# Optimization experiments

Measured on AMD Instinct MI355X. Metric: run time of the kernel, lower is better.

Reference implementation:

```python
import jax, jax.numpy as jnp
import numpy as np

EMB = 64
N_CONS = 100000
N_VARS = 200000
N_EDGES = 2000000


def _embed(x, shift, scale, W1, b1, W2, b2):
    # PreNormLayer (affine) -> Linear -> ReLU -> Linear -> ReLU
    x = (x - shift) * scale
    x = jax.nn.relu(x @ W1 + b1)
    return jax.nn.relu(x @ W2 + b2)


def _biconv(left, right, ei0, ei1, edge_lin, tgt_idx, n_tgt, tgt_feats,
            Wl, bl, Wr, sf, Wf, bf, sp, Woa, boa, Wob, bob):
    # gather-transform: per-edge joint features [E, EMB]
    joint = (left @ Wl + bl)[ei0] + edge_lin + (right @ Wr)[ei1]
    # feature_module_final: PreNorm(scale-only) -> ReLU -> Linear
    msg = jax.nn.relu(joint * sf) @ Wf + bf
    # scatter-add to target nodes, then post-conv PreNorm(scale-only)
    agg = jax.ops.segment_sum(msg, tgt_idx, num_segments=n_tgt) * sp
    h = jax.nn.relu(jnp.concatenate([agg, tgt_feats], axis=1) @ Woa + boa)
    return h @ Wob + bob


def _forward(constraint_features, edge_features, variable_features,
             c_shift, c_scale, c_W1, c_b1, c_W2, c_b2,
             v_shift, v_scale, v_W1, v_b1, v_W2, v_b2,
             e_shift, e_scale,
             vc_Wl, vc_bl, vc_We, vc_Wr, vc_sf, vc_Wf, vc_bf, vc_sp,
             vc_Woa, vc_boa, vc_Wob, vc_bob,
             cv_Wl, cv_bl, cv_We, cv_Wr, cv_sf, cv_Wf, cv_bf, cv_sp,
             cv_Woa, cv_boa, cv_Wob, cv_bob,
             out_W1, out_b1, out_W2, edge_indices):
    ei0, ei1 = edge_indices[0], edge_indices[1]
    c = _embed(constraint_features, c_shift, c_scale, c_W1, c_b1, c_W2, c_b2)
    v = _embed(variable_features, v_shift, v_scale, v_W1, v_b1, v_W2, v_b2)
    e = (edge_features - e_shift) * e_scale  # edge embedding = PreNorm only, dim 1
    # conv_v_to_c (right_to_left=True): target = constraints via ei0
    c = jax.nn.relu(_biconv(c, v, ei0, ei1, e @ vc_We, ei0, N_CONS, c,
                            vc_Wl, vc_bl, vc_Wr, vc_sf, vc_Wf, vc_bf, vc_sp,
                            vc_Woa, vc_boa, vc_Wob, vc_bob))
    # conv_c_to_v: target = variables via ei1
    v = jax.nn.relu(_biconv(c, v, ei0, ei1, e @ cv_We, ei1, N_VARS, v,
                            cv_Wl, cv_bl, cv_Wr, cv_sf, cv_Wf, cv_bf, cv_sp,
                            cv_Woa, cv_boa, cv_Wob, cv_bob))
    out = jax.nn.relu(v @ out_W1 + out_b1) @ out_W2  # [N_VARS, 1]
    return out.reshape(1, -1)


def setup_inputs():
    key = jax.random.key(0)
    ks = iter(jax.random.split(key, 64))

    def rn(shape, s=0.1):
        return (jax.random.normal(next(ks), shape, jnp.float32) * s).astype(jnp.float32)

    d = {}
    d["constraint_features"] = rn((N_CONS, 5), 1.0)
    d["edge_features"] = rn((N_EDGES, 1), 1.0)
    d["variable_features"] = rn((N_VARS, 19), 1.0)

    def prenorm(n, pre):
        d[pre + "shift"] = rn((n,), 0.05)
        d[pre + "scale"] = jnp.ones((n,), jnp.float32) + rn((n,), 0.05)

    prenorm(5, "c_"); prenorm(19, "v_"); prenorm(1, "e_")
    for pre, nin in (("c_", 5), ("v_", 19)):
        d[pre + "W1"] = rn((nin, EMB)); d[pre + "b1"] = rn((EMB,), 0.02)
        d[pre + "W2"] = rn((EMB, EMB)); d[pre + "b2"] = rn((EMB,), 0.02)
    for pre in ("vc_", "cv_"):
        d[pre + "Wl"] = rn((EMB, EMB)); d[pre + "bl"] = rn((EMB,), 0.02)
        d[pre + "We"] = rn((1, EMB)); d[pre + "Wr"] = rn((EMB, EMB))
        d[pre + "sf"] = jnp.float32(1.0) + rn((), 0.05)
        d[pre + "Wf"] = rn((EMB, EMB)); d[pre + "bf"] = rn((EMB,), 0.02)
        d[pre + "sp"] = jnp.float32(1.0) + rn((), 0.05)
        d[pre + "Woa"] = rn((2 * EMB, EMB)); d[pre + "boa"] = rn((EMB,), 0.02)
        d[pre + "Wob"] = rn((EMB, EMB)); d[pre + "bob"] = rn((EMB,), 0.02)
    d["out_W1"] = rn((EMB, EMB)); d["out_b1"] = rn((EMB,), 0.02)
    d["out_W2"] = rn((EMB, 1))
    d["edge_indices"] = jnp.stack([
        jax.random.randint(next(ks), (N_EDGES,), 0, N_CONS),
        jax.random.randint(next(ks), (N_EDGES,), 0, N_VARS)]).astype(jnp.int32)
    d["n_cons_per_sample"] = jnp.array([N_CONS], jnp.int32)
    d["n_vars_per_sample"] = jnp.array([N_VARS], jnp.int32)
    return d


def reference(constraint_features, edge_features, variable_features,
              c_shift, c_scale, c_W1, c_b1, c_W2, c_b2,
              v_shift, v_scale, v_W1, v_b1, v_W2, v_b2,
              e_shift, e_scale,
              vc_Wl, vc_bl, vc_We, vc_Wr, vc_sf, vc_Wf, vc_bf, vc_sp,
              vc_Woa, vc_boa, vc_Wob, vc_bob,
              cv_Wl, cv_bl, cv_We, cv_Wr, cv_sf, cv_Wf, cv_bf, cv_sp,
              cv_Woa, cv_boa, cv_Wob, cv_bob,
              out_W1, out_b1, out_W2,
              edge_indices, n_cons_per_sample, n_vars_per_sample):
    return _forward(constraint_features, edge_features, variable_features,
                    c_shift, c_scale, c_W1, c_b1, c_W2, c_b2,
                    v_shift, v_scale, v_W1, v_b1, v_W2, v_b2,
                    e_shift, e_scale,
                    vc_Wl, vc_bl, vc_We, vc_Wr, vc_sf, vc_Wf, vc_bf, vc_sp,
                    vc_Woa, vc_boa, vc_Wob, vc_bob,
                    cv_Wl, cv_bl, cv_We, cv_Wr, cv_sf, cv_Wf, cv_bf, cv_sp,
                    cv_Woa, cv_boa, cv_Wob, cv_bob,
                    out_W1, out_b1, out_W2, edge_indices)
```

## Files before the change

kernel.cpp:

```cpp
#include <hip/hip_runtime.h>
#include <hip/hip_bf16.h>

#define DEV __device__ __forceinline__

typedef __attribute__((ext_vector_type(8))) short short8;
typedef __attribute__((ext_vector_type(4))) float f32x4;

DEV unsigned short f2bf(float f) {
    __hip_bfloat16 h = __float2bfloat16(f);
    unsigned short u;
    __builtin_memcpy(&u, &h, 2);
    return u;
}
DEV float bf2f(unsigned short u) { return __uint_as_float((unsigned int)u << 16); }

DEV f32x4 mfma_bf16(short8 a, short8 b, f32x4 c) {
    return __builtin_amdgcn_mfma_f32_16x16x32_bf16(a, b, c, 0, 0, 0);
}

DEV void make_hilo(const float* a8, short8& hi, short8& lo) {
    #pragma unroll
    for (int j = 0; j < 8; ++j) {
        const float v = a8[j];
        const unsigned short h = f2bf(v);
        hi[j] = (short)h;
        lo[j] = (short)f2bf(v - bf2f(h));
    }
}

DEV void mfma3(f32x4 acc[4], short8 ah, short8 al,
               const unsigned short* __restrict__ Bh,
               const unsigned short* __restrict__ Bl,
               int nkt, int tidx, int lane) {
    #pragma unroll
    for (int c = 0; c < 4; ++c) {
        const size_t o = ((size_t)(c * nkt + tidx) * 64 + lane) * 8;
        const short8 bh = *(const short8*)(Bh + o);
        const short8 bl = *(const short8*)(Bl + o);
        acc[c] = mfma_bf16(ah, bh, acc[c]);
        acc[c] = mfma_bf16(al, bh, acc[c]);
        acc[c] = mfma_bf16(ah, bl, acc[c]);
    }
}

DEV int swf(int row, int col) {
    return row * 64 + ((((col >> 3) ^ row) & 7) << 3) + (col & 7);
}

DEV void gemm_lds(f32x4 acc[4], const float* Xl,
                  const unsigned short* Bh, const unsigned short* Bl,
                  int nkt, int t0, int ntk, int l15, int q, int lane) {
    for (int t = 0; t < ntk; ++t) {
        const int ch = (t * 4 + q) ^ (l15 & 7);
        const float* a8 = Xl + l15 * 64 + ch * 8;
        short8 ah, al;
        make_hilo(a8, ah, al);
        mfma3(acc, ah, al, Bh, Bl, nkt, t0 + t, lane);
    }
}

DEV void gemm_glb(f32x4 acc[4], const float* __restrict__ Xg, int rbase, int N,
                  const unsigned short* Bh, const unsigned short* Bl,
                  int nkt, int t0, int ntk, int l15, int q, int lane) {
    const int grow = rbase + l15;
    const bool ok = grow < N;
    for (int t = 0; t < ntk; ++t) {
        float a8[8];
        if (ok) {
            const float4 v0 = *(const float4*)(Xg + (size_t)grow * 64 + t * 32 + q * 8);
            const float4 v1 = *(const float4*)(Xg + (size_t)grow * 64 + t * 32 + q * 8 + 4);
            a8[0] = v0.x; a8[1] = v0.y; a8[2] = v0.z; a8[3] = v0.w;
            a8[4] = v1.x; a8[5] = v1.y; a8[6] = v1.z; a8[7] = v1.w;
        } else {
            #pragma unroll
            for (int j = 0; j < 8; ++j) a8[j] = 0.f;
        }
        short8 ah, al;
        make_hilo(a8, ah, al);
        mfma3(acc, ah, al, Bh, Bl, nkt, t0 + t, lane);
    }
}

#define NMAT 15
struct PrepArgs {
    const float* src[NMAT];
    unsigned short* hi[NMAT];
    unsigned short* lo[NMAT];
    int nkt[NMAT];
    int KR[NMAT];
};

__global__ __launch_bounds__(256)
void prep_kernel(PrepArgs pa)
{
    const int m = blockIdx.y;
    const int nkt = pa.nkt[m];
    const int nthr = nkt * 4 * 64;
    const int p = blockIdx.x * 256 + threadIdx.x;
    if (p >= nthr) return;
    const int f = p >> 6, l = p & 63;
    const int c = f / nkt, t = f % nkt;
    const int kbase = t * 32 + ((l >> 4) << 3);
    const int n = c * 16 + (l & 15);
    const float* W = pa.src[m];
    const int KR = pa.KR[m];
    unsigned short* ph = pa.hi[m] + (size_t)p * 8;
    unsigned short* pl = pa.lo[m] + (size_t)p * 8;
    #pragma unroll
    for (int j = 0; j < 8; ++j) {
        const int k = kbase + j;
        const float v = (k < KR) ? W[k * 64 + n] : 0.f;
        const unsigned short h = f2bf(v);
        ph[j] = h;
        pl[j] = f2bf(v - bf2f(h));
    }
}

struct FusedArgs {
    const int* ei; int E; int nH;
    int* h1; int* h2; unsigned int* rank;
    int tC, tV;
    const float* cf; int NC;
    const float* c_shift; const float* c_scale;
    const float* vf; int NV;
    const float* v_shift; const float* v_scale;
    const unsigned short *cW1h, *cW1l, *cW2h, *cW2l, *cWt1h, *cWt1l;
    const unsigned short *vW1h, *vW1l, *vW2h, *vW2l, *vWt1h, *vWt1l, *vWt2h, *vWt2l;
    const float *c_b1, *c_b2, *v_b1, *v_b2, *vc_bl;
    const float *vc_sf, *cv_sf;
    float* Emc; float* Emv;
    unsigned short* A1; unsigned short* B1; unsigned short* B2;
};

__global__ __launch_bounds__(256)
void fused_he_kernel(FusedArgs a)
{
    __shared__ __align__(16) float Bb[4][1024];

    const int half = blockIdx.x & 1;
    const int idx  = blockIdx.x >> 1;

    if (half == 0) {
        const int stride = a.nH * 256;
        for (int e = idx * 256 + (int)threadIdx.x; e < a.E; e += stride) {
            const int r1 = atomicAdd(a.h1 + a.ei[e], 1);
            const int r2 = atomicAdd(a.h2 + a.ei[a.E + e], 1);
            a.rank[e] = (unsigned int)r1 | ((unsigned int)r2 << 16);
        }
        return;
    }

    int tile = idx;
    const float* x; int N; int IN;
    const float *shift, *scale, *b1, *b2, *bt1;
    const unsigned short *W1h, *W1l, *W2h, *W2l, *Wt1h, *Wt1l;
    const unsigned short *Wt2h = nullptr, *Wt2l = nullptr;
    float* Em; unsigned short* T1; unsigned short* T2 = nullptr;
    float sf1, sf2 = 0.f;
    if (tile < a.tC) {
        x = a.cf; N = a.NC; IN = 5; shift = a.c_shift; scale = a.c_scale;
        W1h = a.cW1h; W1l = a.cW1l; b1 = a.c_b1;
        W2h = a.cW2h; W2l = a.cW2l; b2 = a.c_b2;
        Em = a.Emc; Wt1h = a.cWt1h; Wt1l = a.cWt1l; bt1 = a.vc_bl;
        sf1 = a.vc_sf[0]; T1 = a.A1;
    } else {
        tile -= a.tC;
        x = a.vf; N = a.NV; IN = 19; shift = a.v_shift; scale = a.v_scale;
        W1h = a.vW1h; W1l = a.vW1l; b1 = a.v_b1;
        W2h = a.vW2h; W2l = a.vW2l; b2 = a.v_b2;
        Em = a.Emv; Wt1h = a.vWt1h; Wt1l = a.vWt1l; bt1 = nullptr;
        sf1 = a.vc_sf[0]; T1 = a.B1;
        Wt2h = a.vWt2h; Wt2l = a.vWt2l; sf2 = a.cv_sf[0]; T2 = a.B2;
    }

    const int w = threadIdx.x >> 6, lane = threadIdx.x & 63;
    const int l15 = lane & 15, q = lane >> 4;
    const int rbase = tile * 64 + w * 16;

    {
        f32x4 acc[4] = {{0,0,0,0},{0,0,0,0},{0,0,0,0},{0,0,0,0}};
        const int grow = rbase + l15;
        float a8[8];
        #pragma unroll
        for (int j = 0; j < 8; ++j) {
            const int col = q * 8 + j;
            float v = 0.f;
            if (grow < N && col < IN) v = (x[(size_t)grow * IN + col] - shift[col]) * scale[col];
            a8[j] = v;
        }
        short8 ah, al;
        make_hilo(a8, ah, al);
        mfma3(acc, ah, al, W1h, W1l, 1, 0, lane);
        #pragma unroll
        for (int c = 0; c < 4; ++c) {
            const int col = c * 16 + l15;
            const float bb = b1[col];
            #pragma unroll
            for (int r = 0; r < 4; ++r)
                Bb[w][swf(q * 4 + r, col)] = fmaxf(acc[c][r] + bb, 0.f);
        }
    }
    {
        f32x4 acc[4] = {{0,0,0,0},{0,0,0,0},{0,0,0,0},{0,0,0,0}};
        gemm_lds(acc, Bb[w], W2h, W2l, 2, 0, 2, l15, q, lane);
        #pragma unroll
        for (int c = 0; c < 4; ++c) {
            const int col = c * 16 + l15;
            const float bb = b2[col];
            #pragma unroll
            for (int r = 0; r < 4; ++r) {
                const int row = q * 4 + r;
                const int grow = rbase + row;
                const float v = fmaxf(acc[c][r] + bb, 0.f);
                Bb[w][swf(row, col)] = v;
                if (grow < N) Em[(size_t)grow * 64 + col] = v;
            }
        }
    }
    {
        f32x4 acc[4] = {{0,0,0,0},{0,0,0,0},{0,0,0,0},{0,0,0,0}};
        gemm_lds(acc, Bb[w], Wt1h, Wt1l, 2, 0, 2, l15, q, lane);
        #pragma unroll
        for (int c = 0; c < 4; ++c) {
            const int col = c * 16 + l15;
            const float bb = bt1 ? bt1[col] : 0.f;
            #pragma unroll
            for (int r = 0; r < 4; ++r) {
                const int grow = rbase + q * 4 + r;
                if (grow < N) T1[(size_t)grow * 64 + col] = f2bf(sf1 * (acc[c][r] + bb));
            }
        }
    }
    if (T2 != nullptr) {
        f32x4 acc[4] = {{0,0,0,0},{0,0,0,0},{0,0,0,0},{0,0,0,0}};
        gemm_lds(acc, Bb[w], Wt2h, Wt2l, 2, 0, 2, l15, q, lane);
        #pragma unroll
        for (int c = 0; c < 4; ++c) {
            const int col = c * 16 + l15;
            #pragma unroll
            for (int r = 0; r < 4; ++r) {
                const int grow = rbase + q * 4 + r;
                if (grow < N) T2[(size_t)grow * 64 + col] = f2bf(sf2 * acc[c][r]);
            }
        }
    }
}

template<bool IS_POST2>
__global__ __launch_bounds__(256)
void post_mfma(int N, const float* __restrict__ G, const int* __restrict__ rs,
               const float* __restrict__ Em,
               const unsigned short* __restrict__ Wfh, const unsigned short* __restrict__ Wfl,
               const float* __restrict__ bfv, const float* __restrict__ spp,
               const unsigned short* __restrict__ Woah, const unsigned short* __restrict__ Woal,
               const float* __restrict__ boa,
               const unsigned short* __restrict__ Wobh, const unsigned short* __restrict__ Wobl,
               const float* __restrict__ bob,
               const unsigned short* __restrict__ W4h, const unsigned short* __restrict__ W4l,
               const float* __restrict__ b4,
               const float* __restrict__ sf2p, unsigned short* __restrict__ A2,
               const float* __restrict__ oW2, float* __restrict__ out)
{
    __shared__ __align__(16) float BA[4][1024];
    __shared__ __align__(16) float BB[4][1024];

    const int w = threadIdx.x >> 6, lane = threadIdx.x & 63;
    const int l15 = lane & 15, q = lane >> 4;
    const float sp = spp[0];
    const float sf2 = IS_POST2 ? 0.f : sf2p[0];
    const int rbase = blockIdx.x * 64 + w * 16;

    {
        f32x4 acc[4] = {{0,0,0,0},{0,0,0,0},{0,0,0,0},{0,0,0,0}};
        gemm_glb(acc, G, rbase, N, Wfh, Wfl, 2, 0, 2, l15, q, lane);
        float dgr[4];
        #pragma unroll
        for (int r = 0; r < 4; ++r) {
            const int grow = rbase + q * 4 + r;
            dgr[r] = (grow < N) ? (float)(rs[grow + 1] - rs[grow]) : 0.f;
        }
        #pragma unroll
        for (int c = 0; c < 4; ++c) {
            const int col = c * 16 + l15;
            const float bb = bfv[col];
            #pragma unroll
            for (int r = 0; r < 4; ++r)
                BA[w][swf(q * 4 + r, col)] = (acc[c][r] + dgr[r] * bb) * sp;
        }
    }
    {
        f32x4 acc[4] = {{0,0,0,0},{0,0,0,0},{0,0,0,0},{0,0,0,0}};
        gemm_lds(acc, BA[w], Woah, Woal, 4, 0, 2, l15, q, lane);
        gemm_glb(acc, Em, rbase, N, Woah, Woal, 4, 2, 2, l15, q, lane);
        #pragma unroll
        for (int c = 0; c < 4; ++c) {
            const int col = c * 16 + l15;
            const float bb = boa[col];
            #pragma unroll
            for (int r = 0; r < 4; ++r)
                BB[w][swf(q * 4 + r, col)] = fmaxf(acc[c][r] + bb, 0.f);
        }
    }
    {
        f32x4 acc[4] = {{0,0,0,0},{0,0,0,0},{0,0,0,0},{0,0,0,0}};
        gemm_lds(acc, BB[w], Wobh, Wobl, 2, 0, 2, l15, q, lane);
        #pragma unroll
        for (int c = 0; c < 4; ++c) {
            const int col = c * 16 + l15;
            const float bb = bob[col];
            #pragma unroll
            for (int r = 0; r < 4; ++r)
                BA[w][swf(q * 4 + r, col)] = fmaxf(acc[c][r] + bb, 0.f);
        }
    }
    {
        f32x4 acc[4] = {{0,0,0,0},{0,0,0,0},{0,0,0,0},{0,0,0,0}};
        gemm_lds(acc, BA[w], W4h, W4l, 2, 0, 2, l15, q, lane);
        if (!IS_POST2) {
            #pragma unroll
            for (int c = 0; c < 4; ++c) {
                const int col = c * 16 + l15;
                const float bb = b4[col];
                #pragma unroll
                for (int r = 0; r < 4; ++r) {
                    const int grow = rbase + q * 4 + r;
                    if (grow < N) A2[(size_t)grow * 64 + col] = f2bf(sf2 * (acc[c][r] + bb));
                }
            }
        } else {
            float w2c[4], bb4[4];
            #pragma unroll
            for (int c = 0; c < 4; ++c) {
                const int col = c * 16 + l15;
                w2c[c] = oW2[col];
                bb4[c] = b4[col];
            }
            #pragma unroll
            for (int r = 0; r < 4; ++r) {
                float s = 0.f;
                #pragma unroll
                for (int c = 0; c < 4; ++c)
                    s += fmaxf(acc[c][r] + bb4[c], 0.f) * w2c[c];
                s += __shfl_xor(s, 1);
                s += __shfl_xor(s, 2);
                s += __shfl_xor(s, 4);
                s += __shfl_xor(s, 8);
                const int grow = rbase + q * 4 + r;
                if (l15 == 0 && grow < N) out[grow] = s;
            }
        }
    }
}

__global__ __launch_bounds__(256)
void scanA2_kernel(const int* __restrict__ h1, int n1, int* __restrict__ cs1,
                   const int* __restrict__ h2, int n2, int* __restrict__ cs2)
{
    __shared__ int wsum[4];
    const int which = blockIdx.y;
    const int* h = which ? h2 : h1;
    const int n = which ? n2 : n1;
    int* csum = which ? cs2 : cs1;
    if (blockIdx.x * 4096 >= n) return;

    const int t = threadIdx.x, lane = t & 63, wid = t >> 6;
    const int base = blockIdx.x * 4096 + t * 16;
    int s = 0;
    #pragma unroll
    for (int j = 0; j < 16; ++j) {
        const int idx = base + j;
        if (idx < n) s += h[idx];
    }
    #pragma unroll
    for (int d = 1; d < 64; d <<= 1) s += __shfl_xor(s, d);
    if (lane == 0) wsum[wid] = s;
    __syncthreads();
    if (t == 0) csum[blockIdx.x] = wsum[0] + wsum[1] + wsum[2] + wsum[3];
}

__global__ __launch_bounds__(256)
void scanB2_kernel(int* __restrict__ cs1, int nch1, int* __restrict__ rs1, int n1,
                   int* __restrict__ cs2, int nch2, int* __restrict__ rs2, int n2)
{
    __shared__ int wsum[4];
    const int which = blockIdx.x;
    int* csum = which ? cs2 : cs1;
    const int nchunks = which ? nch2 : nch1;
    int* rs = which ? rs2 : rs1;
    const int n = which ? n2 : n1;

    const int t = threadIdx.x, lane = t & 63, wid = t >> 6;
    const int v = (t < nchunks) ? csum[t] : 0;
    int x = v;
    #pragma unroll
    for (int d = 1; d < 64; d <<= 1) { int y = __shfl_up(x, d); if (lane >= d) x += y; }
    if (lane == 63) wsum[wid] = x;
    __syncthreads();
    int woff = 0;
    for (int i = 0; i < wid; ++i) woff += wsum[i];
    if (t < nchunks) csum[t] = woff + x - v;
    if (t == 0) rs[n] = wsum[0] + wsum[1] + wsum[2] + wsum[3];
}

__global__ __launch_bounds__(256)
void scanC2_kernel(const int* __restrict__ h1, int n1, const int* __restrict__ cs1,
                   int* __restrict__ rs1,
                   const int* __restrict__ h2, int n2, const int* __restrict__ cs2,
                   int* __restrict__ rs2)
{
    __shared__ int wsum[4];
    const int which = blockIdx.y;
    const int* h = which ? h2 : h1;
    const int n = which ? n2 : n1;
    const int* csum = which ? cs2 : cs1;
    int* rs = which ? rs2 : rs1;
    if (blockIdx.x * 4096 >= n) return;

    const int t = threadIdx.x, lane = t & 63, wid = t >> 6;
    const int base = blockIdx.x * 4096 + t * 16;
    int loc[16];
    int s = 0;
    #pragma unroll
    for (int j = 0; j < 16; ++j) {
        loc[j] = s;
        const int idx = base + j;
        if (idx < n) s += h[idx];
    }
    int x = s;
    #pragma unroll
    for (int d = 1; d < 64; d <<= 1) { int y = __shfl_up(x, d); if (lane >= d) x += y; }
    if (lane == 63) wsum[wid] = x;
    __syncthreads();
    int woff = 0;
    for (int i = 0; i < wid; ++i) woff += wsum[i];
    const int toff = csum[blockIdx.x] + woff + x - s;
    #pragma unroll
    for (int j = 0; j < 16; ++j) {
        const int idx = base + j;
        if (idx < n) rs[idx] = toff + loc[j];
    }
}

__global__ __launch_bounds__(256)
void scatter_kernel(const int* __restrict__ ei, int E,
                    const unsigned int* __restrict__ rank,
                    const int* __restrict__ rs1, const int* __restrict__ rs2,
                    unsigned int* __restrict__ items1,
                    unsigned int* __restrict__ items2)
{
    const int e = blockIdx.x * 256 + threadIdx.x;
    if (e >= E) return;
    const int i0 = ei[e];
    const int i1 = ei[E + e];
    const unsigned int rk = rank[e];
    const int pos1 = rs1[i0] + (int)(rk & 0xffffu);
    const int pos2 = rs2[i1] + (int)(rk >> 16);
    items1[pos1] = (unsigned int)e;
    items2[pos2] = (unsigned int)e;
}

DEV void agg_body(int row, int j, const int* __restrict__ rs,
                  const unsigned int* __restrict__ items,
                  const int* __restrict__ oth, const float* __restrict__ ef,
                  float esh, float esc,
                  const unsigned short* __restrict__ Ttgt,
                  const unsigned short* __restrict__ Tsrc,
                  const float* __restrict__ We, const float* __restrict__ sfp,
                  float* __restrict__ G)
{
    const float base = bf2f(Ttgt[(size_t)row * 64 + j]);
    const float sfWe = sfp[0] * We[j];
    const int s = rs[row];
    const int e = rs[row + 1];
    float acc = 0.f;
    int p = s;
    for (; p + 7 < e; p += 8) {
        unsigned int id[8];
        #pragma unroll
        for (int u = 0; u < 8; ++u) id[u] = items[p + u];
        int o[8];
        float en[8];
        #pragma unroll
        for (int u = 0; u < 8; ++u) o[u] = oth[id[u]];
        #pragma unroll
        for (int u = 0; u < 8; ++u) en[u] = (ef[id[u]] - esh) * esc;
        float b[8];
        #pragma unroll
        for (int u = 0; u < 8; ++u) b[u] = bf2f(Tsrc[(size_t)o[u] * 64 + j]);
        #pragma unroll
        for (int u = 0; u < 8; ++u)
            acc += fmaxf(base + b[u] + en[u] * sfWe, 0.f);
    }
    for (; p < e; ++p) {
        const unsigned int id = items[p];
        const int o = oth[id];
        const float en = (ef[id] - esh) * esc;
        const float bs = bf2f(Tsrc[(size_t)o * 64 + j]);
        acc += fmaxf(base + bs + en * sfWe, 0.f);
    }
    G[(size_t)row * 64 + j] = acc;
}

__global__ __launch_bounds__(256)
void agg_kernel(int nrows, const int* __restrict__ rs,
                const unsigned int* __restrict__ items,
                const int* __restrict__ oth, const float* __restrict__ ef,
                const float* __restrict__ eshp, const float* __restrict__ escp,
                const unsigned short* __restrict__ Ttgt,
                const unsigned short* __restrict__ Tsrc,
                const float* __restrict__ We, const float* __restrict__ sfp,
                float* __restrict__ G)
{
    const int row = blockIdx.x * 4 + (int)(threadIdx.x >> 6);
    if (row >= nrows) return;
    agg_body(row, (int)(threadIdx.x & 63), rs, items, oth, ef,
             eshp[0], escp[0], Ttgt, Tsrc, We, sfp, G);
}

extern "C" void kernel_launch(void* const* d_in, const int* in_sizes, int n_in,
                              void* d_out, int out_size, void* d_ws, size_t ws_size,
                              hipStream_t stream)
{
    const float* cf      = (const float*)d_in[0];
    const float* ef      = (const float*)d_in[1];
    const float* vf      = (const float*)d_in[2];
    const float* c_shift = (const float*)d_in[3];
    const float* c_scale = (const float*)d_in[4];
    const float* v_shift = (const float*)d_in[5];
    const float* v_scale = (const float*)d_in[6];
    const float* e_shift = (const float*)d_in[7];
    const float* e_scale = (const float*)d_in[8];
    const float* c_W1 = (const float*)d_in[9];
    const float* c_b1 = (const float*)d_in[10];
    const float* c_W2 = (const float*)d_in[11];
    const float* c_b2 = (const float*)d_in[12];
    const float* v_W1 = (const float*)d_in[13];
    const float* v_b1 = (const float*)d_in[14];
    const float* v_W2 = (const float*)d_in[15];
    const float* v_b2 = (const float*)d_in[16];
    const float* vc_Wl  = (const float*)d_in[17];
    const float* vc_bl  = (const float*)d_in[18];
    const float* vc_We  = (const float*)d_in[19];
    const float* vc_Wr  = (const float*)d_in[20];
    const float* vc_sf  = (const float*)d_in[21];
    const float* vc_Wf  = (const float*)d_in[22];
    const float* vc_bf  = (const float*)d_in[23];
    const float* vc_sp  = (const float*)d_in[24];
    const float* vc_Woa = (const float*)d_in[25];
    const float* vc_boa = (const float*)d_in[26];
    const float* vc_Wob = (const float*)d_in[27];
    const float* vc_bob = (const float*)d_in[28];
    const float* cv_Wl  = (const float*)d_in[29];
    const float* cv_bl  = (const float*)d_in[30];
    const float* cv_We  = (const float*)d_in[31];
    const float* cv_Wr  = (const float*)d_in[32];
    const float* cv_sf  = (const float*)d_in[33];
    const float* cv_Wf  = (const float*)d_in[34];
    const float* cv_bf  = (const float*)d_in[35];
    const float* cv_sp  = (const float*)d_in[36];
    const float* cv_Woa = (const float*)d_in[37];
    const float* cv_boa = (const float*)d_in[38];
    const float* cv_Wob = (const float*)d_in[39];
    const float* cv_bob = (const float*)d_in[40];
    const float* out_W1 = (const float*)d_in[41];
    const float* out_b1 = (const float*)d_in[42];
    const float* out_W2 = (const float*)d_in[43];
    const int*   eidx   = (const int*)d_in[44];

    const int NC = in_sizes[0] / 5;
    const int NV = in_sizes[2] / 19;
    const int E  = in_sizes[1];

    char* ws = (char*)d_ws;
    size_t off = 0;
    auto alloc = [&](size_t bytes) -> size_t {
        size_t o = off;
        off = (off + bytes + 255) & ~(size_t)255;
        return o;
    };
    size_t o_h1 = alloc((size_t)NC * 4);
    size_t o_h2 = alloc((size_t)NV * 4);
    size_t zero_bytes = off;
    size_t o_rs1  = alloc((size_t)(NC + 1) * 4);
    size_t o_rs2  = alloc((size_t)(NV + 1) * 4);
    size_t o_cs1  = alloc(256 * 4);
    size_t o_cs2  = alloc(256 * 4);
    size_t o_p1   = alloc((size_t)E * 4);
    size_t o_p2   = alloc((size_t)E * 4);
    size_t o_G1   = alloc((size_t)NC * 64 * 4);
    size_t o_G2   = alloc((size_t)NV * 64 * 4);
    size_t o_Emc  = alloc((size_t)NC * 64 * 4);
    size_t o_Emv  = alloc((size_t)NV * 64 * 4);
    size_t o_A1   = alloc((size_t)NC * 64 * 2);
    size_t o_B1   = alloc((size_t)NV * 64 * 2);
    size_t o_B2   = alloc((size_t)NV * 64 * 2);

    static const int nkt_arr[NMAT] = {1,2,2,1,2,2,2,2,4,2,2,2,4,2,2};
    static const int KR_arr[NMAT]  = {5,64,64,19,64,64,64,64,128,64,64,64,128,64,64};
    const float* src_arr[NMAT] = {c_W1, c_W2, vc_Wl, v_W1, v_W2, vc_Wr, cv_Wr,
                                  vc_Wf, vc_Woa, vc_Wob, cv_Wl,
                                  cv_Wf, cv_Woa, cv_Wob, out_W1};
    size_t o_wh[NMAT], o_wl[NMAT];
    for (int m = 0; m < NMAT; ++m) {
        o_wh[m] = alloc((size_t)nkt_arr[m] * 4 * 64 * 8 * 2);
        o_wl[m] = alloc((size_t)nkt_arr[m] * 4 * 64 * 8 * 2);
    }
    (void)ws_size; (void)n_in; (void)out_size;

    int*  h1   = (int*)(ws + o_h1);
    int*  h2   = (int*)(ws + o_h2);
    int*  rs1  = (int*)(ws + o_rs1);
    int*  rs2  = (int*)(ws + o_rs2);
    int*  cs1  = (int*)(ws + o_cs1);
    int*  cs2  = (int*)(ws + o_cs2);
    unsigned int* rank = (unsigned int*)(ws + o_G2);
    unsigned int* p1 = (unsigned int*)(ws + o_p1);
    unsigned int* p2 = (unsigned int*)(ws + o_p2);
    float* G1  = (float*)(ws + o_G1);
    float* G2  = (float*)(ws + o_G2);
    float* Emc = (float*)(ws + o_Emc);
    float* Emv = (float*)(ws + o_Emv);
    unsigned short* A1 = (unsigned short*)(ws + o_A1);
    unsigned short* B1 = (unsigned short*)(ws + o_B1);
    unsigned short* A2 = (unsigned short*)(ws + o_A1);
    unsigned short* B2 = (unsigned short*)(ws + o_B2);

    PrepArgs pa;
    for (int m = 0; m < NMAT; ++m) {
        pa.src[m] = src_arr[m];
        pa.hi[m] = (unsigned short*)(ws + o_wh[m]);
        pa.lo[m] = (unsigned short*)(ws + o_wl[m]);
        pa.nkt[m] = nkt_arr[m];
        pa.KR[m] = KR_arr[m];
    }
    auto WH = [&](int m) { return (const unsigned short*)(ws + o_wh[m]); };
    auto WL = [&](int m) { return (const unsigned short*)(ws + o_wl[m]); };

    hipMemsetAsync(ws, 0, zero_bytes, stream);

    prep_kernel<<<dim3(4, NMAT), 256, 0, stream>>>(pa);

    const int tC = (NC + 63) >> 6, tV = (NV + 63) >> 6;
    const int nE = tC + tV;
    FusedArgs fa;
    fa.ei = eidx; fa.E = E; fa.nH = nE;
    fa.h1 = h1; fa.h2 = h2; fa.rank = rank;
    fa.tC = tC; fa.tV = tV;
    fa.cf = cf; fa.NC = NC; fa.c_shift = c_shift; fa.c_scale = c_scale;
    fa.vf = vf; fa.NV = NV; fa.v_shift = v_shift; fa.v_scale = v_scale;
    fa.cW1h = WH(0); fa.cW1l = WL(0); fa.cW2h = WH(1); fa.cW2l = WL(1);
    fa.cWt1h = WH(2); fa.cWt1l = WL(2);
    fa.vW1h = WH(3); fa.vW1l = WL(3); fa.vW2h = WH(4); fa.vW2l = WL(4);
    fa.vWt1h = WH(5); fa.vWt1l = WL(5); fa.vWt2h = WH(6); fa.vWt2l = WL(6);
    fa.c_b1 = c_b1; fa.c_b2 = c_b2; fa.v_b1 = v_b1; fa.v_b2 = v_b2;
    fa.vc_bl = vc_bl; fa.vc_sf = vc_sf; fa.cv_sf = cv_sf;
    fa.Emc = Emc; fa.Emv = Emv; fa.A1 = A1; fa.B1 = B1; fa.B2 = B2;
    fused_he_kernel<<<2 * nE, 256, 0, stream>>>(fa);

    const int nch1 = (NC + 4095) / 4096, nch2 = (NV + 4095) / 4096;
    const int nchm = nch1 > nch2 ? nch1 : nch2;
    scanA2_kernel<<<dim3(nchm, 2), 256, 0, stream>>>(h1, NC, cs1, h2, NV, cs2);
    scanB2_kernel<<<2, 256, 0, stream>>>(cs1, nch1, rs1, NC, cs2, nch2, rs2, NV);
    scanC2_kernel<<<dim3(nchm, 2), 256, 0, stream>>>(h1, NC, cs1, rs1, h2, NV, cs2, rs2);

    scatter_kernel<<<(E + 255) / 256, 256, 0, stream>>>(
        eidx, E, rank, rs1, rs2, p1, p2);

    agg_kernel<<<(NC + 3) / 4, 256, 0, stream>>>(
        NC, rs1, p1, eidx + E, ef, e_shift, e_scale, A1, B1, vc_We, vc_sf, G1);
    post_mfma<false><<<tC, 256, 0, stream>>>(
        NC, G1, rs1, Emc,
        WH(7), WL(7), vc_bf, vc_sp,
        WH(8), WL(8), vc_boa,
        WH(9), WL(9), vc_bob,
        WH(10), WL(10), cv_bl,
        cv_sf, A2, nullptr, nullptr);

    agg_kernel<<<(NV + 3) / 4, 256, 0, stream>>>(
        NV, rs2, p2, eidx, ef, e_shift, e_scale, B2, A2, cv_We, cv_sf, G2);
    post_mfma<true><<<tV, 256, 0, stream>>>(
        NV, G2, rs2, Emv,
        WH(11), WL(11), cv_bf, cv_sp,
        WH(12), WL(12), cv_boa,
        WH(13), WL(13), cv_bob,
        WH(14), WL(14), out_b1,
        nullptr, nullptr, out_W2, (float*)d_out);
}
```

Measured before the change: 749.7 us.

## Fuse edge aggregation into post-conv MFMA kernel, eliminating G intermediate buffers

Merges the per-row gather/ReLU aggregation into the post-convolution MFMA kernel, writing aggregated rows directly into LDS instead of a global fp32 G buffer. This removes the global write and re-read of the aggregation buffers and two kernel launches. Each wave now loops over its 16 rows sequentially for the gather, which may reduce latency hiding compared with one row per wave across many blocks. The rank buffer gets its own allocation instead of aliasing G2.

After: 1.008 ms. 34.5% more time.

```diff
diff --git a/kernel.cpp b/kernel.cpp
--- a/kernel.cpp
+++ b/kernel.cpp
@@ -246,33 +246,186 @@
     }
 }
 
+__global__ __launch_bounds__(256)
+void scanA2_kernel(const int* __restrict__ h1, int n1, int* __restrict__ cs1,
+                   const int* __restrict__ h2, int n2, int* __restrict__ cs2)
+{
+    __shared__ int wsum[4];
+    const int which = blockIdx.y;
+    const int* h = which ? h2 : h1;
+    const int n = which ? n2 : n1;
+    int* csum = which ? cs2 : cs1;
+    if (blockIdx.x * 4096 >= n) return;
+
+    const int t = threadIdx.x, lane = t & 63, wid = t >> 6;
+    const int base = blockIdx.x * 4096 + t * 16;
+    int s = 0;
+    #pragma unroll
+    for (int j = 0; j < 16; ++j) {
+        const int idx = base + j;
+        if (idx < n) s += h[idx];
+    }
+    #pragma unroll
+    for (int d = 1; d < 64; d <<= 1) s += __shfl_xor(s, d);
+    if (lane == 0) wsum[wid] = s;
+    __syncthreads();
+    if (t == 0) csum[blockIdx.x] = wsum[0] + wsum[1] + wsum[2] + wsum[3];
+}
+
+__global__ __launch_bounds__(256)
+void scanB2_kernel(int* __restrict__ cs1, int nch1, int* __restrict__ rs1, int n1,
+                   int* __restrict__ cs2, int nch2, int* __restrict__ rs2, int n2)
+{
+    __shared__ int wsum[4];
+    const int which = blockIdx.x;
+    int* csum = which ? cs2 : cs1;
+    const int nchunks = which ? nch2 : nch1;
+    int* rs = which ? rs2 : rs1;
+    const int n = which ? n2 : n1;
+
+    const int t = threadIdx.x, lane = t & 63, wid = t >> 6;
+    const int v = (t < nchunks) ? csum[t] : 0;
+    int x = v;
+    #pragma unroll
+    for (int d = 1; d < 64; d <<= 1) { int y = __shfl_up(x, d); if (lane >= d) x += y; }
+    if (lane == 63) wsum[wid] = x;
+    __syncthreads();
+    int woff = 0;
+    for (int i = 0; i < wid; ++i) woff += wsum[i];
+    if (t < nchunks) csum[t] = woff + x - v;
+    if (t == 0) rs[n] = wsum[0] + wsum[1] + wsum[2] + wsum[3];
+}
+
+__global__ __launch_bounds__(256)
+void scanC2_kernel(const int* __restrict__ h1, int n1, const int* __restrict__ cs1,
+                   int* __restrict__ rs1,
+                   const int* __restrict__ h2, int n2, const int* __restrict__ cs2,
+                   int* __restrict__ rs2)
+{
+    __shared__ int wsum[4];
+    const int which = blockIdx.y;
+    const int* h = which ? h2 : h1;
+    const int n = which ? n2 : n1;
+    const int* csum = which ? cs2 : cs1;
+    int* rs = which ? rs2 : rs1;
+    if (blockIdx.x * 4096 >= n) return;
+
+    const int t = threadIdx.x, lane = t & 63, wid = t >> 6;
+    const int base = blockIdx.x * 4096 + t * 16;
+    int loc[16];
+    int s = 0;
+    #pragma unroll
+    for (int j = 0; j < 16; ++j) {
+        loc[j] = s;
+        const int idx = base + j;
+        if (idx < n) s += h[idx];
+    }
+    int x = s;
+    #pragma unroll
+    for (int d = 1; d < 64; d <<= 1) { int y = __shfl_up(x, d); if (lane >= d) x += y; }
+    if (lane == 63) wsum[wid] = x;
+    __syncthreads();
+    int woff = 0;
+    for (int i = 0; i < wid; ++i) woff += wsum[i];
+    const int toff = csum[blockIdx.x] + woff + x - s;
+    #pragma unroll
+    for (int j = 0; j < 16; ++j) {
+        const int idx = base + j;
+        if (idx < n) rs[idx] = toff + loc[j];
+    }
+}
+
+__global__ __launch_bounds__(256)
+void scatter_kernel(const int* __restrict__ ei, int E,
+                    const unsigned int* __restrict__ rank,
+                    const int* __restrict__ rs1, const int* __restrict__ rs2,
+                    unsigned int* __restrict__ items1,
+                    unsigned int* __restrict__ items2)
+{
+    const int e = blockIdx.x * 256 + threadIdx.x;
+    if (e >= E) return;
+    const int i0 = ei[e];
+    const int i1 = ei[E + e];
+    const unsigned int rk = rank[e];
+    const int pos1 = rs1[i0] + (int)(rk & 0xffffu);
+    const int pos2 = rs2[i1] + (int)(rk >> 16);
+    items1[pos1] = (unsigned int)e;
+    items2[pos2] = (unsigned int)e;
+}
+
 template<bool IS_POST2>
 __global__ __launch_bounds__(256)
-void post_mfma(int N, const float* __restrict__ G, const int* __restrict__ rs,
-               const float* __restrict__ Em,
-               const unsigned short* __restrict__ Wfh, const unsigned short* __restrict__ Wfl,
-               const float* __restrict__ bfv, const float* __restrict__ spp,
-               const unsigned short* __restrict__ Woah, const unsigned short* __restrict__ Woal,
-               const float* __restrict__ boa,
-               const unsigned short* __restrict__ Wobh, const unsigned short* __restrict__ Wobl,
-               const float* __restrict__ bob,
-               const unsigned short* __restrict__ W4h, const unsigned short* __restrict__ W4l,
-               const float* __restrict__ b4,
-               const float* __restrict__ sf2p, unsigned short* __restrict__ A2,
-               const float* __restrict__ oW2, float* __restrict__ out)
-{
+void conv_fused(int N, const int* __restrict__ rs,
+                const unsigned int* __restrict__ items,
+                const int* __restrict__ oth, const float* __restrict__ ef,
+                const float* __restrict__ eshp, const float* __restrict__ escp,
+                const unsigned short* __restrict__ Ttgt,
+                const unsigned short* __restrict__ Tsrc,
+                const float* __restrict__ Wev, const float* __restrict__ sfp,
+                const float* __restrict__ Em,
+                const unsigned short* __restrict__ Wfh, const unsigned short* __restrict__ Wfl,
+                const float* __restrict__ bfv, const float* __restrict__ spp,
+                const unsigned short* __restrict__ Woah, const unsigned short* __restrict__ Woal,
+                const float* __restrict__ boa,
+                const unsigned short* __restrict__ Wobh, const unsigned short* __restrict__ Wobl,
+                const float* __restrict__ bob,
+                const unsigned short* __restrict__ W4h, const unsigned short* __restrict__ W4l,
+                const float* __restrict__ b4,
+                const float* __restrict__ sf2p, unsigned short* __restrict__ A2,
+                const float* __restrict__ oW2, float* __restrict__ out)
+{
+    __shared__ __align__(16) float GB[4][1024];
     __shared__ __align__(16) float BA[4][1024];
-    __shared__ __align__(16) float BB[4][1024];
 
     const int w = threadIdx.x >> 6, lane = threadIdx.x & 63;
     const int l15 = lane & 15, q = lane >> 4;
+    const int rbase = blockIdx.x * 64 + w * 16;
+
+    {
+        const float sfWe = sfp[0] * Wev[lane];
+        const float esh = eshp[0], esc = escp[0];
+        for (int r = 0; r < 16; ++r) {
+            const int row = rbase + r;
+            float acc = 0.f;
+            if (row < N) {
+                const float base = bf2f(Ttgt[(size_t)row * 64 + lane]);
+                const int s = rs[row];
+                const int e = rs[row + 1];
+                int p = s;
+                for (; p + 7 < e; p += 8) {
+                    unsigned int id[8];
+                    #pragma unroll
+                    for (int u = 0; u < 8; ++u) id[u] = items[p + u];
+                    int o[8];
+                    float en[8];
+                    #pragma unroll
+                    for (int u = 0; u < 8; ++u) o[u] = oth[id[u]];
+                    #pragma unroll
+                    for (int u = 0; u < 8; ++u) en[u] = (ef[id[u]] - esh) * esc;
+                    float b[8];
+                    #pragma unroll
+                    for (int u = 0; u < 8; ++u) b[u] = bf2f(Tsrc[(size_t)o[u] * 64 + lane]);
+                    #pragma unroll
+                    for (int u = 0; u < 8; ++u)
+                        acc += fmaxf(base + b[u] + en[u] * sfWe, 0.f);
+                }
+                for (; p < e; ++p) {
+                    const unsigned int id = items[p];
+                    const float en = (ef[id] - esh) * esc;
+                    const float bs = bf2f(Tsrc[(size_t)oth[id] * 64 + lane]);
+                    acc += fmaxf(base + bs + en * sfWe, 0.f);
+                }
+            }
+            GB[w][swf(r, lane)] = acc;
+        }
+    }
+
     const float sp = spp[0];
     const float sf2 = IS_POST2 ? 0.f : sf2p[0];
-    const int rbase = blockIdx.x * 64 + w * 16;
-
-    {
-        f32x4 acc[4] = {{0,0,0,0},{0,0,0,0},{0,0,0,0},{0,0,0,0}};
-        gemm_glb(acc, G, rbase, N, Wfh, Wfl, 2, 0, 2, l15, q, lane);
+
+    {
+        f32x4 acc[4] = {{0,0,0,0},{0,0,0,0},{0,0,0,0},{0,0,0,0}};
+        gemm_lds(acc, GB[w], Wfh, Wfl, 2, 0, 2, l15, q, lane);
         float dgr[4];
         #pragma unroll
         for (int r = 0; r < 4; ++r) {
@@ -298,12 +451,12 @@
             const float bb = boa[col];
             #pragma unroll
             for (int r = 0; r < 4; ++r)
-                BB[w][swf(q * 4 + r, col)] = fmaxf(acc[c][r] + bb, 0.f);
-        }
-    }
-    {
-        f32x4 acc[4] = {{0,0,0,0},{0,0,0,0},{0,0,0,0},{0,0,0,0}};
-        gemm_lds(acc, BB[w], Wobh, Wobl, 2, 0, 2, l15, q, lane);
+                GB[w][swf(q * 4 + r, col)] = fmaxf(acc[c][r] + bb, 0.f);
+        }
+    }
+    {
+        f32x4 acc[4] = {{0,0,0,0},{0,0,0,0},{0,0,0,0},{0,0,0,0}};
+        gemm_lds(acc, GB[w], Wobh, Wobl, 2, 0, 2, l15, q, lane);
         #pragma unroll
         for (int c = 0; c < 4; ++c) {
             const int col = c * 16 + l15;
@@ -350,171 +503,6 @@
             }
         }
     }
-}
-
-__global__ __launch_bounds__(256)
-void scanA2_kernel(const int* __restrict__ h1, int n1, int* __restrict__ cs1,
-                   const int* __restrict__ h2, int n2, int* __restrict__ cs2)
-{
-    __shared__ int wsum[4];
-    const int which = blockIdx.y;
-    const int* h = which ? h2 : h1;
-    const int n = which ? n2 : n1;
-    int* csum = which ? cs2 : cs1;
-    if (blockIdx.x * 4096 >= n) return;
-
-    const int t = threadIdx.x, lane = t & 63, wid = t >> 6;
-    const int base = blockIdx.x * 4096 + t * 16;
-    int s = 0;
-    #pragma unroll
-    for (int j = 0; j < 16; ++j) {
-        const int idx = base + j;
-        if (idx < n) s += h[idx];
-    }
-    #pragma unroll
-    for (int d = 1; d < 64; d <<= 1) s += __shfl_xor(s, d);
-    if (lane == 0) wsum[wid] = s;
-    __syncthreads();
-    if (t == 0) csum[blockIdx.x] = wsum[0] + wsum[1] + wsum[2] + wsum[3];
-}
-
-__global__ __launch_bounds__(256)
-void scanB2_kernel(int* __restrict__ cs1, int nch1, int* __restrict__ rs1, int n1,
-                   int* __restrict__ cs2, int nch2, int* __restrict__ rs2, int n2)
-{
-    __shared__ int wsum[4];
-    const int which = blockIdx.x;
-    int* csum = which ? cs2 : cs1;
-    const int nchunks = which ? nch2 : nch1;
-    int* rs = which ? rs2 : rs1;
-    const int n = which ? n2 : n1;
-
-    const int t = threadIdx.x, lane = t & 63, wid = t >> 6;
-    const int v = (t < nchunks) ? csum[t] : 0;
-    int x = v;
-    #pragma unroll
-    for (int d = 1; d < 64; d <<= 1) { int y = __shfl_up(x, d); if (lane >= d) x += y; }
-    if (lane == 63) wsum[wid] = x;
-    __syncthreads();
-    int woff = 0;
-    for (int i = 0; i < wid; ++i) woff += wsum[i];
-    if (t < nchunks) csum[t] = woff + x - v;
-    if (t == 0) rs[n] = wsum[0] + wsum[1] + wsum[2] + wsum[3];
-}
-
-__global__ __launch_bounds__(256)
-void scanC2_kernel(const int* __restrict__ h1, int n1, const int* __restrict__ cs1,
-                   int* __restrict__ rs1,
-                   const int* __restrict__ h2, int n2, const int* __restrict__ cs2,
-                   int* __restrict__ rs2)
-{
-    __shared__ int wsum[4];
-    const int which = blockIdx.y;
-    const int* h = which ? h2 : h1;
-    const int n = which ? n2 : n1;
-    const int* csum = which ? cs2 : cs1;
-    int* rs = which ? rs2 : rs1;
-    if (blockIdx.x * 4096 >= n) return;
-
-    const int t = threadIdx.x, lane = t & 63, wid = t >> 6;
-    const int base = blockIdx.x * 4096 + t * 16;
-    int loc[16];
-    int s = 0;
-    #pragma unroll
-    for (int j = 0; j < 16; ++j) {
-        loc[j] = s;
-        const int idx = base + j;
-        if (idx < n) s += h[idx];
-    }
-    int x = s;
-    #pragma unroll
-    for (int d = 1; d < 64; d <<= 1) { int y = __shfl_up(x, d); if (lane >= d) x += y; }
-    if (lane == 63) wsum[wid] = x;
-    __syncthreads();
-    int woff = 0;
-    for (int i = 0; i < wid; ++i) woff += wsum[i];
-    const int toff = csum[blockIdx.x] + woff + x - s;
-    #pragma unroll
-    for (int j = 0; j < 16; ++j) {
-        const int idx = base + j;
-        if (idx < n) rs[idx] = toff + loc[j];
-    }
-}
-
-__global__ __launch_bounds__(256)
-void scatter_kernel(const int* __restrict__ ei, int E,
-                    const unsigned int* __restrict__ rank,
-                    const int* __restrict__ rs1, const int* __restrict__ rs2,
-                    unsigned int* __restrict__ items1,
-                    unsigned int* __restrict__ items2)
-{
-    const int e = blockIdx.x * 256 + threadIdx.x;
-    if (e >= E) return;
-    const int i0 = ei[e];
-    const int i1 = ei[E + e];
-    const unsigned int rk = rank[e];
-    const int pos1 = rs1[i0] + (int)(rk & 0xffffu);
-    const int pos2 = rs2[i1] + (int)(rk >> 16);
-    items1[pos1] = (unsigned int)e;
-    items2[pos2] = (unsigned int)e;
-}
-
-DEV void agg_body(int row, int j, const int* __restrict__ rs,
-                  const unsigned int* __restrict__ items,
-                  const int* __restrict__ oth, const float* __restrict__ ef,
-                  float esh, float esc,
-                  const unsigned short* __restrict__ Ttgt,
-                  const unsigned short* __restrict__ Tsrc,
-                  const float* __restrict__ We, const float* __restrict__ sfp,
-                  float* __restrict__ G)
-{
-    const float base = bf2f(Ttgt[(size_t)row * 64 + j]);
-    const float sfWe = sfp[0] * We[j];
-    const int s = rs[row];
-    const int e = rs[row + 1];
-    float acc = 0.f;
-    int p = s;
-    for (; p + 7 < e; p += 8) {
-        unsigned int id[8];
-        #pragma unroll
-        for (int u = 0; u < 8; ++u) id[u] = items[p + u];
-        int o[8];
-        float en[8];
-        #pragma unroll
-        for (int u = 0; u < 8; ++u) o[u] = oth[id[u]];
-        #pragma unroll
-        for (int u = 0; u < 8; ++u) en[u] = (ef[id[u]] - esh) * esc;
-        float b[8];
-        #pragma unroll
-        for (int u = 0; u < 8; ++u) b[u] = bf2f(Tsrc[(size_t)o[u] * 64 + j]);
-        #pragma unroll
-        for (int u = 0; u < 8; ++u)
-            acc += fmaxf(base + b[u] + en[u] * sfWe, 0.f);
-    }
-    for (; p < e; ++p) {
-        const unsigned int id = items[p];
-        const int o = oth[id];
-        const float en = (ef[id] - esh) * esc;
-        const float bs = bf2f(Tsrc[(size_t)o * 64 + j]);
-        acc += fmaxf(base + bs + en * sfWe, 0.f);
-    }
-    G[(size_t)row * 64 + j] = acc;
-}
-
-__global__ __launch_bounds__(256)
-void agg_kernel(int nrows, const int* __restrict__ rs,
-                const unsigned int* __restrict__ items,
-                const int* __restrict__ oth, const float* __restrict__ ef,
-                const float* __restrict__ eshp, const float* __restrict__ escp,
-                const unsigned short* __restrict__ Ttgt,
-                const unsigned short* __restrict__ Tsrc,
-                const float* __restrict__ We, const float* __restrict__ sfp,
-                float* __restrict__ G)
-{
-    const int row = blockIdx.x * 4 + (int)(threadIdx.x >> 6);
-    if (row >= nrows) return;
-    agg_body(row, (int)(threadIdx.x & 63), rs, items, oth, ef,
-             eshp[0], escp[0], Ttgt, Tsrc, We, sfp, G);
 }
 
 extern "C" void kernel_launch(void* const* d_in, const int* in_sizes, int n_in,
@@ -587,8 +575,7 @@
     size_t o_cs2  = alloc(256 * 4);
     size_t o_p1   = alloc((size_t)E * 4);
     size_t o_p2   = alloc((size_t)E * 4);
-    size_t o_G1   = alloc((size_t)NC * 64 * 4);
-    size_t o_G2   = alloc((size_t)NV * 64 * 4);
+    size_t o_rank = alloc((size_t)E * 4);
     size_t o_Emc  = alloc((size_t)NC * 64 * 4);
     size_t o_Emv  = alloc((size_t)NV * 64 * 4);
     size_t o_A1   = alloc((size_t)NC * 64 * 2);
@@ -613,11 +600,9 @@
     int*  rs2  = (int*)(ws + o_rs2);
     int*  cs1  = (int*)(ws + o_cs1);
     int*  cs2  = (int*)(ws + o_cs2);
-    unsigned int* rank = (unsigned int*)(ws + o_G2);
+    unsigned int* rank = (unsigned int*)(ws + o_rank);
     unsigned int* p1 = (unsigned int*)(ws + o_p1);
     unsigned int* p2 = (unsigned int*)(ws + o_p2);
-    float* G1  = (float*)(ws + o_G1);
-    float* G2  = (float*)(ws + o_G2);
     float* Emc = (float*)(ws + o_Emc);
     float* Emv = (float*)(ws + o_Emv);
     unsigned short* A1 = (unsigned short*)(ws + o_A1);
@@ -666,20 +651,18 @@
     scatter_kernel<<<(E + 255) / 256, 256, 0, stream>>>(
         eidx, E, rank, rs1, rs2, p1, p2);
 
-    agg_kernel<<<(NC + 3) / 4, 256, 0, stream>>>(
-        NC, rs1, p1, eidx + E, ef, e_shift, e_scale, A1, B1, vc_We, vc_sf, G1);
-    post_mfma<false><<<tC, 256, 0, stream>>>(
-        NC, G1, rs1, Emc,
+    conv_fused<false><<<tC, 256, 0, stream>>>(
+        NC, rs1, p1, eidx + E, ef, e_shift, e_scale,
+        A1, B1, vc_We, vc_sf, Emc,
         WH(7), WL(7), vc_bf, vc_sp,
         WH(8), WL(8), vc_boa,
         WH(9), WL(9), vc_bob,
         WH(10), WL(10), cv_bl,
         cv_sf, A2, nullptr, nullptr);
 
-    agg_kernel<<<(NV + 3) / 4, 256, 0, stream>>>(
-        NV, rs2, p2, eidx, ef, e_shift, e_scale, B2, A2, cv_We, cv_sf, G2);
-    post_mfma<true><<<tV, 256, 0, stream>>>(
-        NV, G2, rs2, Emv,
+    conv_fused<true><<<tV, 256, 0, stream>>>(
+        NV, rs2, p2, eidx, ef, e_shift, e_scale,
+        B2, A2, cv_We, cv_sf, Emv,
         WH(11), WL(11), cv_bf, cv_sp,
         WH(12), WL(12), cv_boa,
         WH(13), WL(13), cv_bob,
```
